# Kernel optimization log

Measured on AMD Instinct MI355X. Metric: run time of the kernel, lower is better.

The kernel has to match this reference:

```python
import jax, jax.numpy as jnp
import numpy as np
from itertools import product

G = 96          # voxel grid side
B = 2           # batch samples
N_PER = 60000   # occupied voxels per sample
N = B * N_PER
C_IN = 64
C_OUT = 1
NUM_BLOCKS = 2
EPS = 1e-5


def _build_kernel_map():
    """Emulate MinkowskiEngine's coordinate hash map for a k=3, stride=1, 3D conv.
    Returns batch_ids [N], and per-offset (in_idx, out_idx) padded to N with sentinel N."""
    rng = np.random.default_rng(0)
    side = G - 2  # coords in [1, G-2] so offset coords never wrap
    keys_list = []
    for b in range(B):
        lin = rng.choice(side ** 3, size=N_PER, replace=False)
        x = lin // (side * side) + 1
        y = (lin // side) % side + 1
        z = lin % side + 1
        keys_list.append(b * G ** 3 + x * G * G + y * G + z)
    keys = np.concatenate(keys_list)
    batch_ids = np.repeat(np.arange(B), N_PER).astype(np.int32)
    order = np.argsort(keys)
    skeys = keys[order]
    in_idx = np.full((27, N), N, np.int32)   # sentinel N -> zero-padded feature row
    out_idx = np.full((27, N), N, np.int32)  # sentinel N -> dropped output row
    for k, (dx, dy, dz) in enumerate(product((-1, 0, 1), repeat=3)):
        nk = keys + dx * G * G + dy * G + dz  # neighbor coordinate key per output voxel
        pos = np.searchsorted(skeys, nk)
        pc = np.clip(pos, 0, N - 1)
        valid = skeys[pc] == nk
        m = int(valid.sum())
        in_idx[k, :m] = order[pc[valid]]
        out_idx[k, :m] = np.nonzero(valid)[0]
    return batch_ids, in_idx, out_idx


def instance_norm(f, batch_ids, num_batches):
    # per-sample, per-channel normalization over all voxels of each sample (ME InstanceNorm, no affine)
    cnt = jax.ops.segment_sum(jnp.ones((f.shape[0],), f.dtype), batch_ids, num_segments=num_batches)
    mean = jax.ops.segment_sum(f, batch_ids, num_segments=num_batches) / cnt[:, None]
    fc = f - mean[batch_ids]
    var = jax.ops.segment_sum(fc * fc, batch_ids, num_segments=num_batches) / cnt[:, None]
    return fc * jax.lax.rsqrt(var + EPS)[batch_ids]


def sparse_conv(f, w, in_idx, out_idx, bias=None):
    # gather-matmul-scatter per kernel offset; w: [27, Cin, Cout]
    n = f.shape[0]
    fpad = jnp.concatenate([f, jnp.zeros((1, f.shape[1]), f.dtype)], axis=0)
    out = jnp.zeros((n + 1, w.shape[-1]), f.dtype)
    for k in range(w.shape[0]):  # static 27-iteration loop over kernel offsets
        out = out.at[out_idx[k]].add(fpad[in_idx[k]] @ w[k])
    out = out[:n]
    if bias is not None:
        out = out + bias
    return out


def setup_inputs() -> dict:
    batch_ids, in_idx, out_idx = _build_kernel_map()
    key = jax.random.key(0)
    k0, k1, k2, k3 = jax.random.split(key, 4)
    feats = jax.random.normal(k0, (N, C_IN), dtype=jnp.float32)
    w_blocks = jax.random.normal(k1, (NUM_BLOCKS, 2, 27, C_IN, C_IN), dtype=jnp.float32) * 0.02
    w_final = jax.random.normal(k2, (27, C_IN, C_OUT), dtype=jnp.float32) * 0.02
    b_final = jax.random.normal(k3, (C_OUT,), dtype=jnp.float32) * 0.02
    return {
        "feats": feats,
        "w_blocks": w_blocks,
        "w_final": w_final,
        "b_final": b_final,
        "in_idx": jnp.asarray(in_idx),
        "out_idx": jnp.asarray(out_idx),
        "batch_ids": jnp.asarray(batch_ids),
        "batch_size": B,
    }


def reference(feats, w_blocks, w_final, b_final, in_idx, out_idx, batch_ids, batch_size):
    # InstanceNorm + ReLU
    x = jax.nn.relu(instance_norm(feats, batch_ids, batch_size))
    # SparseBasicBlocks: conv -> IN -> relu -> conv -> IN -> +res -> relu
    for b in range(w_blocks.shape[0]):
        res = x
        h = sparse_conv(x, w_blocks[b, 0], in_idx, out_idx)
        h = jax.nn.relu(instance_norm(h, batch_ids, batch_size))
        h = sparse_conv(h, w_blocks[b, 1], in_idx, out_idx)
        h = instance_norm(h, batch_ids, batch_size)
        x = jax.nn.relu(h + res)
    # final conv with bias
    return sparse_conv(x, w_final, in_idx, out_idx, bias=b_final)
```

## Files before the change

### kernel.cpp

```cpp
#include <hip/hip_runtime.h>

#define NPTS 120000
#define NROW 120064
#define NB   60000
#define TAPS 27
#define NBLK (NROW / 128)

typedef short  short8 __attribute__((ext_vector_type(8)));
typedef float  f32x4  __attribute__((ext_vector_type(4)));

__device__ __forceinline__ float bf2f(unsigned short u) {
  unsigned v = ((unsigned)u) << 16;
  float f; __builtin_memcpy(&f, &v, 4); return f;
}
__device__ __forceinline__ unsigned short f2bf(float f) {
  unsigned v; __builtin_memcpy(&v, &f, 4);
  v = v + 0x7FFFu + ((v >> 16) & 1u);
  return (unsigned short)(v >> 16);
}

__global__ __launch_bounds__(256) void k_build_nbr(const int* __restrict__ oi,
                                                   const int* __restrict__ ii,
                                                   int* __restrict__ nbr) {
  int g = blockIdx.x * 256 + threadIdx.x;
  if (g >= TAPS * NPTS) return;
  int o = oi[g];
  if (o < NPTS) nbr[(g / NPTS) * NROW + o] = ii[g];
}

__global__ __launch_bounds__(256) void k_repack(const float* __restrict__ w,
                                                unsigned short* __restrict__ wp) {
  int g = blockIdx.x * 256 + threadIdx.x;
  int e = g & 7, l = (g >> 3) & 63, f = (g >> 9) & 7, rest = g >> 12;
  int t = f >> 1, h = f & 1;
  int kk = h * 32 + (l >> 4) * 8 + e;
  int cc = t * 16 + (l & 15);
  wp[g] = f2bf(w[(rest * 64 + kk) * 64 + cc]);
}

__global__ __launch_bounds__(256) void k_stats1_f32(const float* __restrict__ F,
                                                    float* __restrict__ P) {
  int lane = threadIdx.x & 63, wave = threadIdx.x >> 6;
  int batch = blockIdx.x >> 7, bb = blockIdx.x & 127;
  const float* Fb = F + (size_t)batch * NB * 64;
  float s = 0.f, ss = 0.f;
  for (int r = bb * 4 + wave; r < NB; r += 512) {
    float v = Fb[(size_t)r * 64 + lane];
    s += v; ss += v * v;
  }
  __shared__ float ls[4][64], lss[4][64];
  ls[wave][lane] = s; lss[wave][lane] = ss;
  __syncthreads();
  if (threadIdx.x < 64) {
    float S  = ls[0][lane] + ls[1][lane] + ls[2][lane] + ls[3][lane];
    float SS = lss[0][lane] + lss[1][lane] + lss[2][lane] + lss[3][lane];
    P[blockIdx.x * 128 + lane]      = S;
    P[blockIdx.x * 128 + 64 + lane] = SS;
  }
}

__global__ void k_stats2(const float* __restrict__ P, float* __restrict__ MRS) {
  int t = threadIdx.x;
  if (t >= 128) return;
  int b = t >> 6, c = t & 63;
  float S = 0.f, SS = 0.f;
  for (int blk = 0; blk < 128; ++blk) {
    S  += P[(b * 128 + blk) * 128 + c];
    SS += P[(b * 128 + blk) * 128 + 64 + c];
  }
  float mean = S * (1.f / NB);
  float var  = SS * (1.f / NB) - mean * mean;
  MRS[b * 128 + c]      = mean;
  MRS[b * 128 + 64 + c] = rsqrtf(var + 1e-5f);
}

__global__ void k_stats2f(const float* __restrict__ P, float* __restrict__ MRS) {
  int t = threadIdx.x;
  float S = 0.f;
  for (int blk = 0; blk < NBLK; ++blk) S += P[(size_t)blk * 256 + t];
  __shared__ float sm[256];
  sm[t] = S;
  __syncthreads();
  if (t < 128) {
    int b = t >> 6, c = t & 63;
    float mean = sm[(b * 2 + 0) * 64 + c] * (1.f / NB);
    float var  = sm[(b * 2 + 1) * 64 + c] * (1.f / NB) - mean * mean;
    MRS[b * 128 + c]      = mean;
    MRS[b * 128 + 64 + c] = rsqrtf(var + 1e-5f);
  }
}

__global__ __launch_bounds__(256) void k_apply_f2b(const float* __restrict__ F,
                                                   const float* __restrict__ MRS,
                                                   unsigned short* __restrict__ O) {
  int i = blockIdx.x * 256 + threadIdx.x;
  int r = i >> 3, cb = (i & 7) * 8;
  int b = (r >= NB) ? 1 : 0;
  f32x4 v0 = *((const f32x4*)F + i * 2);
  f32x4 v1 = *((const f32x4*)F + i * 2 + 1);
  short8 o;
#pragma unroll
  for (int e = 0; e < 4; ++e) {
    float f = (v0[e] - MRS[b * 128 + cb + e]) * MRS[b * 128 + 64 + cb + e];
    o[e] = (short)f2bf(fmaxf(f, 0.f));
    float g = (v1[e] - MRS[b * 128 + cb + 4 + e]) * MRS[b * 128 + 64 + cb + 4 + e];
    o[e + 4] = (short)f2bf(fmaxf(g, 0.f));
  }
  *((short8*)O + i) = o;
}

__global__ __launch_bounds__(256) void k_apply_bf(const unsigned short* __restrict__ F,
                                                  const float* __restrict__ MRS,
                                                  unsigned short* __restrict__ O) {
  int i = blockIdx.x * 256 + threadIdx.x;
  int r = i >> 3, cb = (i & 7) * 8;
  int b = (r >= NB) ? 1 : 0;
  short8 v = *((const short8*)F + i);
  short8 o;
#pragma unroll
  for (int e = 0; e < 8; ++e) {
    float f = bf2f((unsigned short)v[e]);
    f = (f - MRS[b * 128 + cb + e]) * MRS[b * 128 + 64 + cb + e];
    o[e] = (short)f2bf(fmaxf(f, 0.f));
  }
  *((short8*)O + i) = o;
}

__global__ __launch_bounds__(256) void k_apply_res_bf(const unsigned short* __restrict__ H2,
                                                      const float* __restrict__ MRS,
                                                      unsigned short* __restrict__ X) {
  int i = blockIdx.x * 256 + threadIdx.x;
  int r = i >> 3, cb = (i & 7) * 8;
  int b = (r >= NB) ? 1 : 0;
  short8 v = *((const short8*)H2 + i);
  short8 xv = *((const short8*)X + i);
  short8 o;
#pragma unroll
  for (int e = 0; e < 8; ++e) {
    float f = bf2f((unsigned short)v[e]);
    f = (f - MRS[b * 128 + cb + e]) * MRS[b * 128 + 64 + cb + e];
    f += bf2f((unsigned short)xv[e]);
    o[e] = (short)f2bf(fmaxf(f, 0.f));
  }
  *((short8*)X + i) = o;
}

__global__ __launch_bounds__(256) void k_conv64s(const unsigned short* __restrict__ X,
                                                 const unsigned short* __restrict__ WP,
                                                 const int* __restrict__ nbr,
                                                 unsigned short* __restrict__ Y,
                                                 float* __restrict__ P) {
  const int lane = threadIdx.x & 63, wave = threadIdx.x >> 6;
  const int j0w = blockIdx.x * 128 + wave * 32;
  const int lrow = lane & 15, lk = lane >> 4;
  f32x4 acc[2][4];
#pragma unroll
  for (int g = 0; g < 2; ++g)
#pragma unroll
    for (int c = 0; c < 4; ++c) acc[g][c] = (f32x4){0.f, 0.f, 0.f, 0.f};

  for (int k = 0; k < TAPS; ++k) {
    const int* np = nbr + (size_t)k * NROW + j0w + lrow;
    int i0 = np[0], i1 = np[16];
    if (__ballot(i0 >= 0 || i1 >= 0) == 0ull) continue;
    short8 a00 = {0,0,0,0,0,0,0,0}, a01 = {0,0,0,0,0,0,0,0};
    short8 a10 = {0,0,0,0,0,0,0,0}, a11 = {0,0,0,0,0,0,0,0};
    if (i0 >= 0) {
      const unsigned short* rp = X + (size_t)i0 * 64 + lk * 8;
      a00 = *(const short8*)rp; a01 = *(const short8*)(rp + 32);
    }
    if (i1 >= 0) {
      const unsigned short* rp = X + (size_t)i1 * 64 + lk * 8;
      a10 = *(const short8*)rp; a11 = *(const short8*)(rp + 32);
    }
    const unsigned short* wpk = WP + k * 4096 + lane * 8;
#pragma unroll
    for (int ct = 0; ct < 4; ++ct) {
      short8 b0 = *(const short8*)(wpk + ct * 1024);
      short8 b1 = *(const short8*)(wpk + ct * 1024 + 512);
      acc[0][ct] = __builtin_amdgcn_mfma_f32_16x16x32_bf16(a00, b0, acc[0][ct], 0, 0, 0);
      acc[0][ct] = __builtin_amdgcn_mfma_f32_16x16x32_bf16(a01, b1, acc[0][ct], 0, 0, 0);
      acc[1][ct] = __builtin_amdgcn_mfma_f32_16x16x32_bf16(a10, b0, acc[1][ct], 0, 0, 0);
      acc[1][ct] = __builtin_amdgcn_mfma_f32_16x16x32_bf16(a11, b1, acc[1][ct], 0, 0, 0);
    }
  }
#pragma unroll
  for (int g = 0; g < 2; ++g) {
    unsigned short* yp = Y + (size_t)(j0w + g * 16 + lk * 4) * 64 + lrow;
#pragma unroll
    for (int r = 0; r < 4; ++r) {
      yp[r * 64 +  0] = f2bf(acc[g][0][r]);
      yp[r * 64 + 16] = f2bf(acc[g][1][r]);
      yp[r * 64 + 32] = f2bf(acc[g][2][r]);
      yp[r * 64 + 48] = f2bf(acc[g][3][r]);
    }
  }
  float s[4][2], q[4][2];
#pragma unroll
  for (int ct = 0; ct < 4; ++ct) { s[ct][0] = s[ct][1] = q[ct][0] = q[ct][1] = 0.f; }
#pragma unroll
  for (int g = 0; g < 2; ++g) {
    int rowbase = j0w + g * 16 + lk * 4;
#pragma unroll
    for (int r = 0; r < 4; ++r) {
      int bt = (rowbase + r) >= NB;
#pragma unroll
      for (int ct = 0; ct < 4; ++ct) {
        float v = acc[g][ct][r];
        s[ct][bt] += v; q[ct][bt] += v * v;
      }
    }
  }
  __shared__ float sred[4][4][4][64];
#pragma unroll
  for (int ct = 0; ct < 4; ++ct)
#pragma unroll
    for (int b = 0; b < 2; ++b) {
      sred[wave][lk][b * 2 + 0][ct * 16 + lrow] = s[ct][b];
      sred[wave][lk][b * 2 + 1][ct * 16 + lrow] = q[ct][b];
    }
  __syncthreads();
  int t = threadIdx.x;
  float S = 0.f;
#pragma unroll
  for (int w = 0; w < 4; ++w)
#pragma unroll
    for (int l2 = 0; l2 < 4; ++l2)
      S += sred[w][l2][t >> 6][t & 63];
  P[(size_t)blockIdx.x * 256 + t] = S;
}

__global__ __launch_bounds__(256) void k_dfin(const unsigned short* __restrict__ X,
                                              const float* __restrict__ WF,
                                              float* __restrict__ D) {
  const int lane = threadIdx.x & 63, wave = threadIdx.x >> 6;
  const int j0 = blockIdx.x * 64 + wave * 16;
  const int lrow = lane & 15, lk = lane >> 4;
  const unsigned short* rp = X + (size_t)(j0 + lrow) * 64 + lk * 8;
  short8 a0 = *(const short8*)rp;
  short8 a1 = *(const short8*)(rp + 32);
  short8 b[2][2];
#pragma unroll
  for (int ct = 0; ct < 2; ++ct) {
    int col = ct * 16 + lrow;
#pragma unroll
    for (int h = 0; h < 2; ++h) {
#pragma unroll
      for (int e = 0; e < 8; ++e)
        b[ct][h][e] = (col < TAPS) ? (short)f2bf(WF[col * 64 + h * 32 + lk * 8 + e]) : (short)0;
    }
  }
  f32x4 acc0 = {0,0,0,0}, acc1 = {0,0,0,0};
  acc0 = __builtin_amdgcn_mfma_f32_16x16x32_bf16(a0, b[0][0], acc0, 0, 0, 0);
  acc0 = __builtin_amdgcn_mfma_f32_16x16x32_bf16(a1, b[0][1], acc0, 0, 0, 0);
  acc1 = __builtin_amdgcn_mfma_f32_16x16x32_bf16(a0, b[1][0], acc1, 0, 0, 0);
  acc1 = __builtin_amdgcn_mfma_f32_16x16x32_bf16(a1, b[1][1], acc1, 0, 0, 0);
  float* dp0 = D + (size_t)lrow * NROW + j0 + lk * 4;
  float* dp1 = D + (size_t)(16 + lrow) * NROW + j0 + lk * 4;
#pragma unroll
  for (int r = 0; r < 4; ++r) { dp0[r] = acc0[r]; dp1[r] = acc1[r]; }
}

__global__ __launch_bounds__(256) void k_gfin(const float* __restrict__ D,
                                              const int* __restrict__ nbr,
                                              const float* __restrict__ BF,
                                              float* __restrict__ out) {
  int j = blockIdx.x * 256 + threadIdx.x;
  if (j >= NPTS) return;
  float acc = BF[0];
#pragma unroll
  for (int k = 0; k < TAPS; ++k) {
    int idx = nbr[(size_t)k * NROW + j];
    if (idx >= 0) acc += D[(size_t)k * NROW + idx];
  }
  out[j] = acc;
}

extern "C" void kernel_launch(void* const* d_in, const int* in_sizes, int n_in,
                              void* d_out, int out_size, void* d_ws, size_t ws_size,
                              hipStream_t stream) {
  (void)in_sizes; (void)n_in; (void)out_size; (void)ws_size;
  const float* feats = (const float*)d_in[0];
  const float* wblk  = (const float*)d_in[1];
  const float* wfin  = (const float*)d_in[2];
  const float* bfin  = (const float*)d_in[3];
  const int* in_idx  = (const int*)d_in[4];
  const int* out_idx = (const int*)d_in[5];

  char* p = (char*)d_ws;
  size_t off = 0;
  auto carve = [&](size_t bytes) {
    void* r = p + off; off += (bytes + 255) & ~(size_t)255; return r;
  };
  int*            nbr = (int*)carve((size_t)TAPS * NROW * 4);
  unsigned short* Xb  = (unsigned short*)carve((size_t)NROW * 64 * 2);
  unsigned short* Hb  = (unsigned short*)carve((size_t)NROW * 64 * 2);
  unsigned short* H2b = (unsigned short*)carve((size_t)NROW * 64 * 2);
  unsigned short* WP  = (unsigned short*)carve(108u * 4096u * 2);
  float*          D   = (float*)carve((size_t)32 * NROW * 4);
  float*          P   = (float*)carve(256 * 128 * 4);
  float*          P2  = (float*)carve((size_t)NBLK * 256 * 4);
  float*          MRS = (float*)carve(256 * 4);

  hipMemsetAsync(nbr, 0xFF, (size_t)TAPS * NROW * 4, stream);
  k_build_nbr<<<(TAPS * NPTS + 255) / 256, 256, 0, stream>>>(out_idx, in_idx, nbr);
  k_repack<<<1728, 256, 0, stream>>>(wblk, WP);

  k_stats1_f32<<<256, 256, 0, stream>>>(feats, P);
  k_stats2<<<1, 128, 0, stream>>>(P, MRS);
  k_apply_f2b<<<3750, 256, 0, stream>>>(feats, MRS, Xb);

  k_conv64s<<<NBLK, 256, 0, stream>>>(Xb, WP + 0 * 110592, nbr, Hb, P2);
  k_stats2f<<<1, 256, 0, stream>>>(P2, MRS);
  k_apply_bf<<<3750, 256, 0, stream>>>(Hb, MRS, Hb);
  k_conv64s<<<NBLK, 256, 0, stream>>>(Hb, WP + 1 * 110592, nbr, H2b, P2);
  k_stats2f<<<1, 256, 0, stream>>>(P2, MRS);
  k_apply_res_bf<<<3750, 256, 0, stream>>>(H2b, MRS, Xb);

  k_conv64s<<<NBLK, 256, 0, stream>>>(Xb, WP + 2 * 110592, nbr, Hb, P2);
  k_stats2f<<<1, 256, 0, stream>>>(P2, MRS);
  k_apply_bf<<<3750, 256, 0, stream>>>(Hb, MRS, Hb);
  k_conv64s<<<NBLK, 256, 0, stream>>>(Hb, WP + 3 * 110592, nbr, H2b, P2);
  k_stats2f<<<1, 256, 0, stream>>>(P2, MRS);
  k_apply_res_bf<<<3750, 256, 0, stream>>>(H2b, MRS, Xb);

  k_dfin<<<NROW / 64, 256, 0, stream>>>(Xb, wfin, D);
  k_gfin<<<NROW / 256, 256, 0, stream>>>(D, nbr, bfin, (float*)d_out);
}
```

Baseline: 524.5 us.

## Double-buffer conv gathers with zero-row padding and atomic stats reduction

The conv kernel now prefetches the next tap's neighbor rows while running MFMAs on the current tap. Missing neighbors point at an appended zero row, so the branchy skip logic and the per-tap ballot are gone. The separate single-block stats-finalize kernels are removed: blocks atomically add partial sums into zeroed buffers, and the apply kernels compute mean and rstd inline. This saves five serial launches and hides gather latency, at the cost of doing every tap even when all neighbors are empty, plus more registers and float-atomic nondeterminism.

```diff
diff --git a/kernel.cpp b/kernel.cpp
--- a/kernel.cpp
+++ b/kernel.cpp
@@ -39,7 +39,7 @@
 }
 
 __global__ __launch_bounds__(256) void k_stats1_f32(const float* __restrict__ F,
-                                                    float* __restrict__ P) {
+                                                    float* __restrict__ SM) {
   int lane = threadIdx.x & 63, wave = threadIdx.x >> 6;
   int batch = blockIdx.x >> 7, bb = blockIdx.x & 127;
   const float* Fb = F + (size_t)batch * NB * 64;
@@ -54,44 +54,13 @@
   if (threadIdx.x < 64) {
     float S  = ls[0][lane] + ls[1][lane] + ls[2][lane] + ls[3][lane];
     float SS = lss[0][lane] + lss[1][lane] + lss[2][lane] + lss[3][lane];
-    P[blockIdx.x * 128 + lane]      = S;
-    P[blockIdx.x * 128 + 64 + lane] = SS;
-  }
-}
-
-__global__ void k_stats2(const float* __restrict__ P, float* __restrict__ MRS) {
-  int t = threadIdx.x;
-  if (t >= 128) return;
-  int b = t >> 6, c = t & 63;
-  float S = 0.f, SS = 0.f;
-  for (int blk = 0; blk < 128; ++blk) {
-    S  += P[(b * 128 + blk) * 128 + c];
-    SS += P[(b * 128 + blk) * 128 + 64 + c];
-  }
-  float mean = S * (1.f / NB);
-  float var  = SS * (1.f / NB) - mean * mean;
-  MRS[b * 128 + c]      = mean;
-  MRS[b * 128 + 64 + c] = rsqrtf(var + 1e-5f);
-}
-
-__global__ void k_stats2f(const float* __restrict__ P, float* __restrict__ MRS) {
-  int t = threadIdx.x;
-  float S = 0.f;
-  for (int blk = 0; blk < NBLK; ++blk) S += P[(size_t)blk * 256 + t];
-  __shared__ float sm[256];
-  sm[t] = S;
-  __syncthreads();
-  if (t < 128) {
-    int b = t >> 6, c = t & 63;
-    float mean = sm[(b * 2 + 0) * 64 + c] * (1.f / NB);
-    float var  = sm[(b * 2 + 1) * 64 + c] * (1.f / NB) - mean * mean;
-    MRS[b * 128 + c]      = mean;
-    MRS[b * 128 + 64 + c] = rsqrtf(var + 1e-5f);
+    atomicAdd(&SM[(batch * 2 + 0) * 64 + lane], S);
+    atomicAdd(&SM[(batch * 2 + 1) * 64 + lane], SS);
   }
 }
 
 __global__ __launch_bounds__(256) void k_apply_f2b(const float* __restrict__ F,
-                                                   const float* __restrict__ MRS,
+                                                   const float* __restrict__ SM,
                                                    unsigned short* __restrict__ O) {
   int i = blockIdx.x * 256 + threadIdx.x;
   int r = i >> 3, cb = (i & 7) * 8;
@@ -100,17 +69,18 @@
   f32x4 v1 = *((const f32x4*)F + i * 2 + 1);
   short8 o;
 #pragma unroll
-  for (int e = 0; e < 4; ++e) {
-    float f = (v0[e] - MRS[b * 128 + cb + e]) * MRS[b * 128 + 64 + cb + e];
-    o[e] = (short)f2bf(fmaxf(f, 0.f));
-    float g = (v1[e] - MRS[b * 128 + cb + 4 + e]) * MRS[b * 128 + 64 + cb + 4 + e];
-    o[e + 4] = (short)f2bf(fmaxf(g, 0.f));
+  for (int e = 0; e < 8; ++e) {
+    float mean = SM[(b * 2 + 0) * 64 + cb + e] * (1.f / NB);
+    float var  = SM[(b * 2 + 1) * 64 + cb + e] * (1.f / NB) - mean * mean;
+    float rstd = rsqrtf(var + 1e-5f);
+    float x = (e < 4) ? v0[e & 3] : v1[e & 3];
+    o[e] = (short)f2bf(fmaxf((x - mean) * rstd, 0.f));
   }
   *((short8*)O + i) = o;
 }
 
 __global__ __launch_bounds__(256) void k_apply_bf(const unsigned short* __restrict__ F,
-                                                  const float* __restrict__ MRS,
+                                                  const float* __restrict__ SM,
                                                   unsigned short* __restrict__ O) {
   int i = blockIdx.x * 256 + threadIdx.x;
   int r = i >> 3, cb = (i & 7) * 8;
@@ -119,15 +89,17 @@
   short8 o;
 #pragma unroll
   for (int e = 0; e < 8; ++e) {
-    float f = bf2f((unsigned short)v[e]);
-    f = (f - MRS[b * 128 + cb + e]) * MRS[b * 128 + 64 + cb + e];
+    float mean = SM[(b * 2 + 0) * 64 + cb + e] * (1.f / NB);
+    float var  = SM[(b * 2 + 1) * 64 + cb + e] * (1.f / NB) - mean * mean;
+    float rstd = rsqrtf(var + 1e-5f);
+    float f = (bf2f((unsigned short)v[e]) - mean) * rstd;
     o[e] = (short)f2bf(fmaxf(f, 0.f));
   }
   *((short8*)O + i) = o;
 }
 
 __global__ __launch_bounds__(256) void k_apply_res_bf(const unsigned short* __restrict__ H2,
-                                                      const float* __restrict__ MRS,
+                                                      const float* __restrict__ SM,
                                                       unsigned short* __restrict__ X) {
   int i = blockIdx.x * 256 + threadIdx.x;
   int r = i >> 3, cb = (i & 7) * 8;
@@ -137,9 +109,10 @@
   short8 o;
 #pragma unroll
   for (int e = 0; e < 8; ++e) {
-    float f = bf2f((unsigned short)v[e]);
-    f = (f - MRS[b * 128 + cb + e]) * MRS[b * 128 + 64 + cb + e];
-    f += bf2f((unsigned short)xv[e]);
+    float mean = SM[(b * 2 + 0) * 64 + cb + e] * (1.f / NB);
+    float var  = SM[(b * 2 + 1) * 64 + cb + e] * (1.f / NB) - mean * mean;
+    float rstd = rsqrtf(var + 1e-5f);
+    float f = (bf2f((unsigned short)v[e]) - mean) * rstd + bf2f((unsigned short)xv[e]);
     o[e] = (short)f2bf(fmaxf(f, 0.f));
   }
   *((short8*)X + i) = o;
@@ -149,41 +122,51 @@
                                                  const unsigned short* __restrict__ WP,
                                                  const int* __restrict__ nbr,
                                                  unsigned short* __restrict__ Y,
-                                                 float* __restrict__ P) {
+                                                 float* __restrict__ SM) {
   const int lane = threadIdx.x & 63, wave = threadIdx.x >> 6;
   const int j0w = blockIdx.x * 128 + wave * 32;
   const int lrow = lane & 15, lk = lane >> 4;
+  const int nb0 = j0w + lrow;
   f32x4 acc[2][4];
 #pragma unroll
   for (int g = 0; g < 2; ++g)
 #pragma unroll
     for (int c = 0; c < 4; ++c) acc[g][c] = (f32x4){0.f, 0.f, 0.f, 0.f};
 
-  for (int k = 0; k < TAPS; ++k) {
-    const int* np = nbr + (size_t)k * NROW + j0w + lrow;
+  short8 aA[2][2], aB[2][2];
+
+  auto GATHER = [&](int k, short8 (&a)[2][2]) {
+    const int* np = nbr + (size_t)k * NROW + nb0;
     int i0 = np[0], i1 = np[16];
-    if (__ballot(i0 >= 0 || i1 >= 0) == 0ull) continue;
-    short8 a00 = {0,0,0,0,0,0,0,0}, a01 = {0,0,0,0,0,0,0,0};
-    short8 a10 = {0,0,0,0,0,0,0,0}, a11 = {0,0,0,0,0,0,0,0};
-    if (i0 >= 0) {
-      const unsigned short* rp = X + (size_t)i0 * 64 + lk * 8;
-      a00 = *(const short8*)rp; a01 = *(const short8*)(rp + 32);
-    }
-    if (i1 >= 0) {
-      const unsigned short* rp = X + (size_t)i1 * 64 + lk * 8;
-      a10 = *(const short8*)rp; a11 = *(const short8*)(rp + 32);
-    }
+    const unsigned short* r0 = X + (size_t)(i0 >= 0 ? i0 : NROW) * 64 + lk * 8;
+    const unsigned short* r1 = X + (size_t)(i1 >= 0 ? i1 : NROW) * 64 + lk * 8;
+    a[0][0] = *(const short8*)r0; a[0][1] = *(const short8*)(r0 + 32);
+    a[1][0] = *(const short8*)r1; a[1][1] = *(const short8*)(r1 + 32);
+  };
+  auto TAP = [&](int k, short8 (&a)[2][2]) {
     const unsigned short* wpk = WP + k * 4096 + lane * 8;
 #pragma unroll
     for (int ct = 0; ct < 4; ++ct) {
       short8 b0 = *(const short8*)(wpk + ct * 1024);
       short8 b1 = *(const short8*)(wpk + ct * 1024 + 512);
-      acc[0][ct] = __builtin_amdgcn_mfma_f32_16x16x32_bf16(a00, b0, acc[0][ct], 0, 0, 0);
-      acc[0][ct] = __builtin_amdgcn_mfma_f32_16x16x32_bf16(a01, b1, acc[0][ct], 0, 0, 0);
-      acc[1][ct] = __builtin_amdgcn_mfma_f32_16x16x32_bf16(a10, b0, acc[1][ct], 0, 0, 0);
-      acc[1][ct] = __builtin_amdgcn_mfma_f32_16x16x32_bf16(a11, b1, acc[1][ct], 0, 0, 0);
-    }
-  }
+      acc[0][ct] = __builtin_amdgcn_mfma_f32_16x16x32_bf16(a[0][0], b0, acc[0][ct], 0, 0, 0);
+      acc[0][ct] = __builtin_amdgcn_mfma_f32_16x16x32_bf16(a[0][1], b1, acc[0][ct], 0, 0, 0);
+      acc[1][ct] = __builtin_amdgcn_mfma_f32_16x16x32_bf16(a[1][0], b0, acc[1][ct], 0, 0, 0);
+      acc[1][ct] = __builtin_amdgcn_mfma_f32_16x16x32_bf16(a[1][1], b1, acc[1][ct], 0, 0, 0);
+    }
+  };
+
+  GATHER(0, aA);
+#pragma unroll
+  for (int kk = 0; kk < TAPS; kk += 2) {
+    if (kk + 1 < TAPS) GATHER(kk + 1, aB);
+    TAP(kk, aA);
+    if (kk + 1 < TAPS) {
+      if (kk + 2 < TAPS) GATHER(kk + 2, aA);
+      TAP(kk + 1, aB);
+    }
+  }
+
 #pragma unroll
   for (int g = 0; g < 2; ++g) {
     unsigned short* yp = Y + (size_t)(j0w + g * 16 + lk * 4) * 64 + lrow;
@@ -195,6 +178,7 @@
       yp[r * 64 + 48] = f2bf(acc[g][3][r]);
     }
   }
+
   float s[4][2], q[4][2];
 #pragma unroll
   for (int ct = 0; ct < 4; ++ct) { s[ct][0] = s[ct][1] = q[ct][0] = q[ct][1] = 0.f; }
@@ -227,7 +211,7 @@
 #pragma unroll
     for (int l2 = 0; l2 < 4; ++l2)
       S += sred[w][l2][t >> 6][t & 63];
-  P[(size_t)blockIdx.x * 256 + t] = S;
+  atomicAdd(&SM[t], S);
 }
 
 __global__ __launch_bounds__(256) void k_dfin(const unsigned short* __restrict__ X,
@@ -293,36 +277,38 @@
     void* r = p + off; off += (bytes + 255) & ~(size_t)255; return r;
   };
   int*            nbr = (int*)carve((size_t)TAPS * NROW * 4);
-  unsigned short* Xb  = (unsigned short*)carve((size_t)NROW * 64 * 2);
-  unsigned short* Hb  = (unsigned short*)carve((size_t)NROW * 64 * 2);
+  unsigned short* Xb  = (unsigned short*)carve((size_t)(NROW + 1) * 64 * 2);
+  unsigned short* Hb  = (unsigned short*)carve((size_t)(NROW + 1) * 64 * 2);
   unsigned short* H2b = (unsigned short*)carve((size_t)NROW * 64 * 2);
   unsigned short* WP  = (unsigned short*)carve(108u * 4096u * 2);
   float*          D   = (float*)carve((size_t)32 * NROW * 4);
-  float*          P   = (float*)carve(256 * 128 * 4);
-  float*          P2  = (float*)carve((size_t)NBLK * 256 * 4);
-  float*          MRS = (float*)carve(256 * 4);
+  float*          SMa = (float*)carve(5 * 256 * 4);
+
+  float* SM0 = SMa;
+  float* SM1 = SMa + 256;
+  float* SM2 = SMa + 512;
+  float* SM3 = SMa + 768;
+  float* SM4 = SMa + 1024;
 
   hipMemsetAsync(nbr, 0xFF, (size_t)TAPS * NROW * 4, stream);
+  hipMemsetAsync(SMa, 0, 5 * 256 * 4, stream);
+  hipMemsetAsync(Xb + (size_t)NROW * 64, 0, 128, stream);
+  hipMemsetAsync(Hb + (size_t)NROW * 64, 0, 128, stream);
   k_build_nbr<<<(TAPS * NPTS + 255) / 256, 256, 0, stream>>>(out_idx, in_idx, nbr);
   k_repack<<<1728, 256, 0, stream>>>(wblk, WP);
 
-  k_stats1_f32<<<256, 256, 0, stream>>>(feats, P);
-  k_stats2<<<1, 128, 0, stream>>>(P, MRS);
-  k_apply_f2b<<<3750, 256, 0, stream>>>(feats, MRS, Xb);
-
-  k_conv64s<<<NBLK, 256, 0, stream>>>(Xb, WP + 0 * 110592, nbr, Hb, P2);
-  k_stats2f<<<1, 256, 0, stream>>>(P2, MRS);
-  k_apply_bf<<<3750, 256, 0, stream>>>(Hb, MRS, Hb);
-  k_conv64s<<<NBLK, 256, 0, stream>>>(Hb, WP + 1 * 110592, nbr, H2b, P2);
-  k_stats2f<<<1, 256, 0, stream>>>(P2, MRS);
-  k_apply_res_bf<<<3750, 256, 0, stream>>>(H2b, MRS, Xb);
-
-  k_conv64s<<<NBLK, 256, 0, stream>>>(Xb, WP + 2 * 110592, nbr, Hb, P2);
-  k_stats2f<<<1, 256, 0, stream>>>(P2, MRS);
-  k_apply_bf<<<3750, 256, 0, stream>>>(Hb, MRS, Hb);
-  k_conv64s<<<NBLK, 256, 0, stream>>>(Hb, WP + 3 * 110592, nbr, H2b, P2);
-  k_stats2f<<<1, 256, 0, stream>>>(P2, MRS);
-  k_apply_res_bf<<<3750, 256, 0, stream>>>(H2b, MRS, Xb);
+  k_stats1_f32<<<256, 256, 0, stream>>>(feats, SM0);
+  k_apply_f2b<<<3750, 256, 0, stream>>>(feats, SM0, Xb);
+
+  k_conv64s<<<NBLK, 256, 0, stream>>>(Xb, WP + 0 * 110592, nbr, Hb, SM1);
+  k_apply_bf<<<3750, 256, 0, stream>>>(Hb, SM1, Hb);
+  k_conv64s<<<NBLK, 256, 0, stream>>>(Hb, WP + 1 * 110592, nbr, H2b, SM2);
+  k_apply_res_bf<<<3750, 256, 0, stream>>>(H2b, SM2, Xb);
+
+  k_conv64s<<<NBLK, 256, 0, stream>>>(Xb, WP + 2 * 110592, nbr, Hb, SM3);
+  k_apply_bf<<<3750, 256, 0, stream>>>(Hb, SM3, Hb);
+  k_conv64s<<<NBLK, 256, 0, stream>>>(Hb, WP + 3 * 110592, nbr, H2b, SM4);
+  k_apply_res_bf<<<3750, 256, 0, stream>>>(H2b, SM4, Xb);
 
   k_dfin<<<NROW / 64, 256, 0, stream>>>(Xb, wfin, D);
   k_gfin<<<NROW / 256, 256, 0, stream>>>(D, nbr, bfin, (float*)d_out);
```

Result: faster. 451.4 us (-13.9%).
